# Performance work log

Measured on AMD Instinct MI355X. Metric: run time of the kernel, lower is better.

## Reference

```python
import jax, jax.numpy as jnp
from jax import lax
import numpy as np

DN = ('NCHW', 'OIHW', 'NCHW')
DL = 64
B = 1024


def _cbr(x, w, g, b, stride, pad):
    """Conv2d(bias=False) -> BatchNorm2d (training stats, eps=1e-5) -> ReLU."""
    y = lax.conv_general_dilated(x, w, (stride, stride), [(pad, pad), (pad, pad)],
                                 dimension_numbers=DN)
    m = y.mean(axis=(0, 2, 3), keepdims=True)
    v = ((y - m) ** 2).mean(axis=(0, 2, 3), keepdims=True)  # biased var, as torch BN
    y = (y - m) * lax.rsqrt(v + 1e-5)
    return jax.nn.relu(y * g[None, :, None, None] + b[None, :, None, None])


def setup_inputs() -> dict:
    key = jax.random.key(0)
    ks = jax.random.split(key, 7)
    dl = DL
    inp = {
        'x': jax.random.normal(ks[0], (B, 3, 32, 32), jnp.float32),
        'w1': jax.random.normal(ks[1], (32, 3, 3, 3), jnp.float32) * 0.1,
        'w2': jax.random.normal(ks[2], (64, 32, 3, 3), jnp.float32) * 0.05,
        'w3': jax.random.normal(ks[3], (64, 64, 3, 3), jnp.float32) * 0.05,
        'wa': jax.random.normal(ks[4], (dl, 32, 1, 1), jnp.float32) * 0.1,
        'ws1': jax.random.normal(ks[5], (3 * dl, 32, 3, 3), jnp.float32) * 0.05,
        'ws2': jax.random.normal(ks[6], (3 * dl, 3 * dl, 3, 3), jnp.float32) * 0.03,
    }
    for i, c in enumerate([32, 64, 64, dl, 3 * dl, 3 * dl]):
        inp[f'g{i}'] = jnp.ones((c,), jnp.float32)
        inp[f'b{i}'] = jnp.zeros((c,), jnp.float32)
    return inp


def _encoder(x, w1, w2, w3, wa, ws1, ws2,
             g0, b0, g1, b1, g2, b2, g3, b3, g4, b4, g5, b5):
    dl = DL
    h = _cbr(x, w1, g0, b0, 1, 1)            # [B, 32, 32, 32]
    h = _cbr(h, w2, g1, b1, 1, 1)            # [B, 64, 32, 32]
    AS = _cbr(h, w3, g2, b2, 2, 1)           # [B, 64, 16, 16]
    A_, S_ = jnp.split(AS, 2, axis=1)        # each [B, 32, 16, 16]
    A = _cbr(A_, wa, g3, b3, 1, 0)           # [B, dl, 16, 16]
    S = _cbr(S_, ws1, g4, b4, 1, 1)          # [B, 3dl, 16, 16]
    S = _cbr(S, ws2, g5, b5, 2, 1)           # [B, 3dl, 8, 8]
    b, _, ps, _ = S.shape
    S = S.reshape(b, dl, 3, ps, ps)

    # per-sample conv_transpose2d(A[ii] [1,dl,pa,pa], weight S[ii] [dl,3,ps,ps],
    # stride=2, padding=3) expressed as lhs-dilated cross-correlation with
    # flipped, channel-swapped kernel; batched via vmap (no Python loop).
    pad = ps - 1 - 3  # k - 1 - torch_padding = 4

    def ct(a, s):  # a: [dl,16,16], s: [dl,3,8,8]
        wt = jnp.flip(s, (-2, -1)).transpose(1, 0, 2, 3)  # [3, dl, 8, 8]
        return lax.conv_general_dilated(a[None], wt, (1, 1),
                                        [(pad, pad), (pad, pad)],
                                        lhs_dilation=(2, 2),
                                        dimension_numbers=DN)[0]

    recon = jax.vmap(ct)(A, S)               # [B, 3, 32, 32]
    img = jax.nn.sigmoid(x)
    recon = jax.nn.sigmoid(recon)
    l1 = jnp.mean((img - recon) ** 2)
    l2 = jnp.mean(jax.nn.relu(S))
    logp = jax.nn.log_softmax(S, axis=1)     # softmax over dl axis (dim=1)
    l3 = -jnp.mean(jnp.exp(logp) * logp)
    return A, S, 0.1 * l1, 0.1 * l2, 0.1 * l3


def reference(x, w1, w2, w3, wa, ws1, ws2,
              g0, b0, g1, b1, g2, b2, g3, b3, g4, b4, g5, b5):
    return _encoder(x, w1, w2, w3, wa, ws1, ws2,
                    g0, b0, g1, b1, g2, b2, g3, b3, g4, b4, g5, b5)
```

## Files before the change

kernel.cpp:

```cpp
#include <hip/hip_runtime.h>
#include <math.h>


typedef __attribute__((ext_vector_type(8))) short short8v;
typedef __attribute__((ext_vector_type(4))) short short4v;
typedef __attribute__((ext_vector_type(4))) float f32x4;

__device__ __forceinline__ unsigned short f2bf(float f) {
  union { float f; unsigned u; } a; a.f = f;
  unsigned r = a.u + 0x7fffu + ((a.u >> 16) & 1u);
  return (unsigned short)(r >> 16);
}
__device__ __forceinline__ float bf2f(unsigned short h) {
  union { unsigned u; float f; } a; a.u = ((unsigned)h) << 16;
  return a.f;
}

__device__ __forceinline__ float wave_reduce(float v) {
#pragma unroll
  for (int off = 32; off; off >>= 1) v += __shfl_down(v, off, 64);
  return v;
}

template <int CI, int CO>
__device__ __forceinline__ void reord1(const float* __restrict__ w,
                                       unsigned short* __restrict__ wr,
                                       int idx) {
  int e = idx & 7;
  int t = idx >> 3;
  int co = t % CO; t /= CO;
  int ci8 = t % (CI / 8);
  int kk = t / (CI / 8);
  int ci = ci8 * 8 + e;
  wr[idx] = f2bf(w[((size_t)co * CI + ci) * 9 + kk]);
}

__global__ __launch_bounds__(256) void wreord_all_k(
    const float* __restrict__ w2, const float* __restrict__ w3,
    const float* __restrict__ ws1, const float* __restrict__ ws2,
    unsigned short* __restrict__ w2r, unsigned short* __restrict__ w3r,
    unsigned short* __restrict__ ws1r, unsigned short* __restrict__ ws2r) {
  int idx = blockIdx.x * 256 + threadIdx.x;
  if (idx < 18432) reord1<32, 64>(w2, w2r, idx);
  else if (idx < 55296) reord1<64, 64>(w3, w3r, idx - 18432);
  else if (idx < 110592) reord1<32, 192>(ws1, ws1r, idx - 55296);
  else if (idx < 442368) reord1<192, 192>(ws2, ws2r, idx - 110592);
}

__global__ __launch_bounds__(256) void conv0_k(const float* __restrict__ in,
                                               const float* __restrict__ w,
                                               unsigned short* __restrict__ outB,
                                               double* __restrict__ part) {
  __shared__ __align__(16) float tile[3][34][36];
  const int b = blockIdx.x;
  const int co0 = blockIdx.y * 8;
  const int tid = threadIdx.x;
  const int row = tid >> 3, x0 = (tid & 7) * 4;
  const int wv = tid >> 6;

  float* tf = &tile[0][0][0];
  for (int i = tid; i < 918; i += 256)
    *(float4*)(tf + i * 4) = make_float4(0.f, 0.f, 0.f, 0.f);
  __syncthreads();
  for (int i = tid; i < 768; i += 256) {
    int x4 = i & 7, yy = (i >> 3) & 31, c = i >> 8;
    float4 v = *(const float4*)&in[(((size_t)b * 3 + c) * 32 + yy) * 32 + x4 * 4];
    float* dst = &tile[c][yy + 1][1 + x4 * 4];
    dst[0] = v.x; dst[1] = v.y; dst[2] = v.z; dst[3] = v.w;
  }
  __syncthreads();

  float acc[4][8];
#pragma unroll
  for (int p = 0; p < 4; ++p)
#pragma unroll
    for (int co = 0; co < 8; ++co) acc[p][co] = 0.f;

#pragma unroll
  for (int c = 0; c < 3; ++c)
#pragma unroll
    for (int ky = 0; ky < 3; ++ky) {
      const float* tr = &tile[c][row + ky][x0];
      float4 vlo = *(const float4*)tr;
      float2 vhi = *(const float2*)(tr + 4);
      float v[6] = {vlo.x, vlo.y, vlo.z, vlo.w, vhi.x, vhi.y};
#pragma unroll
      for (int kx = 0; kx < 3; ++kx)
#pragma unroll
        for (int co = 0; co < 8; ++co) {
          float wvv = w[((size_t)(co0 + co) * 3 + c) * 9 + ky * 3 + kx];
#pragma unroll
          for (int p = 0; p < 4; ++p)
            acc[p][co] = fmaf(v[p + kx], wvv, acc[p][co]);
        }
    }
#pragma unroll
  for (int p = 0; p < 4; ++p) {
    short8v o;
#pragma unroll
    for (int co = 0; co < 8; ++co) o[co] = (short)f2bf(acc[p][co]);
    *(short8v*)&outB[(((size_t)b * 32 + row) * 32 + x0 + p) * 32 + co0] = o;
  }

  float s8[8], q8[8];
#pragma unroll
  for (int co = 0; co < 8; ++co) {
    float s = 0.f, q = 0.f;
#pragma unroll
    for (int p = 0; p < 4; ++p) {
      float v = acc[p][co];
      s += v;
      q = fmaf(v, v, q);
    }
    s8[co] = wave_reduce(s);
    q8[co] = wave_reduce(q);
  }
  __syncthreads();
  float* sb = (float*)tile;
  if ((tid & 63) == 0) {
#pragma unroll
    for (int co = 0; co < 8; ++co) {
      sb[wv * 8 + co] = s8[co];
      sb[32 + wv * 8 + co] = q8[co];
    }
  }
  __syncthreads();
  if (tid < 8) {
    float S = 0.f, Q = 0.f;
#pragma unroll
    for (int k = 0; k < 4; ++k) {
      S += sb[k * 8 + tid];
      Q += sb[32 + k * 8 + tid];
    }
    size_t slot = ((size_t)(co0 + tid) * 1024 + b) * 2;
    part[slot] = (double)S;
    part[slot + 1] = (double)Q;
  }
}

template <int CI_T, int CI0, int CI, int CIP, int CO, int COB, int IHW,
          int OHW, int STRIDE, int ORPB, int WM, int WN, int CTM, int CTN,
          bool OUT_BF16T>
__global__ __launch_bounds__(512) void convgemm_k(
    const unsigned short* __restrict__ inT, const float* __restrict__ ss,
    const unsigned short* __restrict__ wr_w, float* __restrict__ outF,
    unsigned short* __restrict__ outB, double* __restrict__ part) {
  constexpr int IR = (ORPB - 1) * STRIDE + 3;
  constexpr int IW2 = IHW + 2;
  constexpr int NPX = ORPB * OHW;
  constexpr int NPIX = OHW * OHW;
  constexpr bool SWZ = (STRIDE == 2);
  static_assert(WM * WN == 8, "8 waves");
  static_assert(WN * CTN * 16 == NPX, "px tiling");
  static_assert(WM * CTM * 16 == COB, "co tiling");
  static_assert((IR * IW2 * CIP) % 4 == 0, "zero fill");
  static_assert(IR * IW2 * CIP * 2 >= 8 * CTM * 16 * 2 * 4, "stats overlay");
  static_assert(!SWZ || (CI / 8) % 8 == 0, "swizzle octet closure");
  __shared__ __align__(16) unsigned short st[IR * IW2 * CIP];

  const int b = blockIdx.x;
  const int oy0 = blockIdx.y * ORPB;
  const int co_base = blockIdx.z * COB;
  const int tid = threadIdx.x;
  const int w = tid >> 6, l = tid & 63;
  const int l16 = l & 15, g = l >> 4;
  const int wrow = w / WN, wcol = w % WN;

  {
    uint2 z = make_uint2(0u, 0u);
    uint2* stz = (uint2*)st;
    constexpr int NZ = IR * IW2 * CIP / 4;
    for (int i = tid; i < NZ; i += 512) stz[i] = z;
  }
  __syncthreads();

  {
    constexpr int CPP = CI / 8;
    constexpr int NCH = IR * IHW * CPP;
    const int r0in = oy0 * STRIDE - 1;
    for (int i = tid; i < NCH; i += 512) {
      int c8 = i % CPP;
      int xx = (i / CPP) % IHW;
      int ir = i / (CPP * IHW);
      int iy = r0in + ir;
      if ((unsigned)iy < (unsigned)IHW) {
        short8v raw = *(const short8v*)&inT[(((size_t)b * IHW + iy) * IHW + xx) *
                                            CI_T + CI0 + c8 * 8];
        f32x4 sc0 = *(const f32x4*)&ss[CI0 + c8 * 8];
        f32x4 sc1 = *(const f32x4*)&ss[CI0 + c8 * 8 + 4];
        f32x4 sh0 = *(const f32x4*)&ss[CI_T + CI0 + c8 * 8];
        f32x4 sh1 = *(const f32x4*)&ss[CI_T + CI0 + c8 * 8 + 4];
        short4v lo, hi;
#pragma unroll
        for (int e = 0; e < 4; ++e) {
          float f = bf2f((unsigned short)raw[e]);
          f = fmaxf(fmaf(f, sc0[e], sh0[e]), 0.f);
          lo[e] = (short)f2bf(f);
        }
#pragma unroll
        for (int e = 0; e < 4; ++e) {
          float f = bf2f((unsigned short)raw[e + 4]);
          f = fmaxf(fmaf(f, sc1[e], sh1[e]), 0.f);
          hi[e] = (short)f2bf(f);
        }
        int xcol = xx + 1;
        int gran = SWZ ? (c8 ^ (xcol & 7)) : c8;
        unsigned short* dst = &st[(ir * IW2 + xcol) * CIP + gran * 8];
        *(short4v*)dst = lo;
        *(short4v*)(dst + 4) = hi;
      }
    }
  }
  __syncthreads();

  int prow[CTN], pxx[CTN];
#pragma unroll
  for (int pn = 0; pn < CTN; ++pn) {
    int pxl = (wcol * CTN + pn) * 16 + l16;
    int ly = pxl / OHW, lx = pxl % OHW;
    prow[pn] = (ly * STRIDE * IW2 + lx * STRIDE) * CIP;
    pxx[pn] = lx * STRIDE;
  }
  const int co_off = co_base + wrow * CTM * 16 + l16;

  f32x4 acc[CTM][CTN];
#pragma unroll
  for (int cm = 0; cm < CTM; ++cm)
#pragma unroll
    for (int pn = 0; pn < CTN; ++pn) {
      f32x4 z = {0.f, 0.f, 0.f, 0.f};
      acc[cm][pn] = z;
    }

#pragma unroll 3
  for (int kk = 0; kk < 9; ++kk) {
    const int ky = kk / 3, kx = kk % 3;
    const int rowadd = (ky * IW2 + kx) * CIP;
#pragma unroll
    for (int cs = 0; cs < CI / 32; ++cs) {
      short8v bfr[CTN];
#pragma unroll
      for (int pn = 0; pn < CTN; ++pn) {
        int gran = cs * 4 + g;
        if (SWZ) gran ^= ((pxx[pn] + kx) & 7);
        const unsigned short* bp = &st[prow[pn] + rowadd + gran * 8];
        short4v lo = *(const short4v*)bp;
        short4v hi = *(const short4v*)(bp + 4);
        short8v v = {lo[0], lo[1], lo[2], lo[3], hi[0], hi[1], hi[2], hi[3]};
        bfr[pn] = v;
      }
      const unsigned short* wb =
          wr_w + ((size_t)(kk * (CI / 8) + cs * 4 + g) * CO + co_off) * 8;
      short8v afr[CTM];
#pragma unroll
      for (int cm = 0; cm < CTM; ++cm)
        afr[cm] = *(const short8v*)(wb + cm * 128);
#pragma unroll
      for (int cm = 0; cm < CTM; ++cm)
#pragma unroll
        for (int pn = 0; pn < CTN; ++pn)
          acc[cm][pn] = __builtin_amdgcn_mfma_f32_16x16x32_bf16(
              afr[cm], bfr[pn], acc[cm][pn], 0, 0, 0);
    }
  }

#pragma unroll
  for (int cm = 0; cm < CTM; ++cm)
#pragma unroll
    for (int pn = 0; pn < CTN; ++pn) {
      int pxl = (wcol * CTN + pn) * 16 + l16;
      size_t pxg = (size_t)oy0 * OHW + pxl;
      int co = co_base + (wrow * CTM + cm) * 16 + g * 4;
      if (OUT_BF16T) {
        unsigned d0 = (unsigned)f2bf(acc[cm][pn][0]) |
                      ((unsigned)f2bf(acc[cm][pn][1]) << 16);
        unsigned d1 = (unsigned)f2bf(acc[cm][pn][2]) |
                      ((unsigned)f2bf(acc[cm][pn][3]) << 16);
        unsigned* dst = (unsigned*)&outB[((size_t)b * NPIX + pxg) * CO + co];
        dst[0] = d0;
        dst[1] = d1;
      } else {
#pragma unroll
        for (int r = 0; r < 4; ++r)
          outF[((size_t)b * CO + co + r) * NPIX + pxg] = acc[cm][pn][r];
      }
    }

  float sst[CTM][4], qst[CTM][4];
#pragma unroll
  for (int cm = 0; cm < CTM; ++cm)
#pragma unroll
    for (int r = 0; r < 4; ++r) {
      float s = 0.f, q = 0.f;
#pragma unroll
      for (int pn = 0; pn < CTN; ++pn) {
        float v = acc[cm][pn][r];
        s += v;
        q = fmaf(v, v, q);
      }
#pragma unroll
      for (int mask = 1; mask < 16; mask <<= 1) {
        s += __shfl_xor(s, mask, 64);
        q += __shfl_xor(q, mask, 64);
      }
      sst[cm][r] = s;
      qst[cm][r] = q;
    }
  __syncthreads();
  float* sbuf = (float*)st;
  float* qbuf = sbuf + 8 * CTM * 16;
  if (l16 == 0) {
#pragma unroll
    for (int cm = 0; cm < CTM; ++cm)
#pragma unroll
      for (int r = 0; r < 4; ++r) {
        sbuf[((w * CTM + cm) * 4 + g) * 4 + r] = sst[cm][r];
        qbuf[((w * CTM + cm) * 4 + g) * 4 + r] = qst[cm][r];
      }
  }
  __syncthreads();
  if (tid < COB) {
    int wrow_t = tid / (CTM * 16);
    int rem = tid % (CTM * 16);
    float S = 0.f, Q = 0.f;
#pragma unroll
    for (int j = 0; j < WN; ++j) {
      int wvx = wrow_t * WN + j;
      S += sbuf[(wvx * CTM) * 16 + rem];
      Q += qbuf[(wvx * CTM) * 16 + rem];
    }
    const int blk = blockIdx.x * gridDim.y + blockIdx.y;
    const int nblk = 1024 * gridDim.y;
    size_t slot = ((size_t)(co_base + tid) * nblk + blk) * 2;
    part[slot] = (double)S;
    part[slot + 1] = (double)Q;
  }
}

__global__ __launch_bounds__(256) void finalize_k(
    const double* __restrict__ part, int NB, const float* __restrict__ g,
    const float* __restrict__ bb, float* __restrict__ ss, int C, double invN) {
  __shared__ double sms[256], smq[256];
  const int c = blockIdx.x;
  const int t = threadIdx.x;
  double s = 0.0, q = 0.0;
  const double* base = part + (size_t)c * NB * 2;
  for (int i = t; i < NB; i += 256) {
    s += base[i * 2];
    q += base[i * 2 + 1];
  }
  sms[t] = s;
  smq[t] = q;
  __syncthreads();
  for (int st = 128; st; st >>= 1) {
    if (t < st) {
      sms[t] += sms[t + st];
      smq[t] += smq[t + st];
    }
    __syncthreads();
  }
  if (t == 0) {
    double mean = sms[0] * invN;
    double var = smq[0] * invN - mean * mean;
    float scale = g[c] * rsqrtf((float)var + 1e-5f);
    float shift = bb[c] - (float)mean * scale;
    ss[c] = scale;
    ss[C + c] = shift;
  }
}

__global__ __launch_bounds__(256) void norm_relu_k(float* __restrict__ y,
                                                   const float* __restrict__ ss,
                                                   int C, int HW, long total) {
  long stride = (long)gridDim.x * 256 * 4;
  for (long i = ((long)blockIdx.x * 256 + threadIdx.x) * 4; i < total;
       i += stride) {
    int c = (int)((i / HW) % C);
    float sc = ss[c], sh = ss[C + c];
    float4 v = *(const float4*)(y + i);
    v.x = fmaxf(fmaf(v.x, sc, sh), 0.f);
    v.y = fmaxf(fmaf(v.y, sc, sh), 0.f);
    v.z = fmaxf(fmaf(v.z, sc, sh), 0.f);
    v.w = fmaxf(fmaf(v.w, sc, sh), 0.f);
    *(float4*)(y + i) = v;
  }
}

__global__ __launch_bounds__(256) void conv1x1_k(
    const unsigned short* __restrict__ inT, const float* __restrict__ ss,
    const float* __restrict__ w, float* __restrict__ out,
    double* __restrict__ part) {
  __shared__ float sb1x[4][16], qb1x[4][16];
  const int b = blockIdx.x;
  const int co0 = blockIdx.y * 16;
  const int px = threadIdx.x;
  const int wv = threadIdx.x >> 6;
  float acc[16];
#pragma unroll
  for (int co = 0; co < 16; ++co) acc[co] = 0.f;
  const unsigned short* rowp = inT + ((size_t)b * 256 + px) * 64;
#pragma unroll
  for (int c8 = 0; c8 < 4; ++c8) {
    short8v raw = *(const short8v*)(rowp + c8 * 8);
#pragma unroll
    for (int e = 0; e < 8; ++e) {
      int c = c8 * 8 + e;
      float f = bf2f((unsigned short)raw[e]);
      f = fmaxf(fmaf(f, ss[c], ss[64 + c]), 0.f);
#pragma unroll
      for (int co = 0; co < 16; ++co)
        acc[co] = fmaf(f, w[(co0 + co) * 32 + c], acc[co]);
    }
  }
#pragma unroll
  for (int co = 0; co < 16; ++co)
    out[((size_t)b * 64 + co0 + co) * 256 + px] = acc[co];

#pragma unroll
  for (int co = 0; co < 16; ++co) {
    float s = wave_reduce(acc[co]);
    float q = wave_reduce(acc[co] * acc[co]);
    if ((threadIdx.x & 63) == 0) {
      sb1x[wv][co] = s;
      qb1x[wv][co] = q;
    }
  }
  __syncthreads();
  if (px < 16) {
    float S = 0.f, Q = 0.f;
#pragma unroll
    for (int k = 0; k < 4; ++k) {
      S += sb1x[k][px];
      Q += qb1x[k][px];
    }
    size_t slot = ((size_t)(co0 + px) * 1024 + b) * 2;
    part[slot] = (double)S;
    part[slot + 1] = (double)Q;
  }
}

__global__ __launch_bounds__(256) void convt_l1_k(const float* __restrict__ A,
                                                  const float* __restrict__ S,
                                                  const float* __restrict__ x,
                                                  double* __restrict__ l1p) {
  __shared__ unsigned short Ab[8][256][8];
  __shared__ unsigned short Sb[4][16][3][72];
  __shared__ float sbred[4];
  const int b = blockIdx.x, tid = threadIdx.x;
  const int w = tid >> 6, l = tid & 63;
  const int g = l >> 4, c = l & 15;
  const int pa = w >> 1, pb = w & 1;

  const float* Ag = A + (size_t)b * 16384;
  for (int dp = 0; dp < 32; ++dp) {
    int d = dp * 2;
    unsigned lo = f2bf(Ag[(size_t)d * 256 + tid]);
    unsigned hi = f2bf(Ag[(size_t)(d + 1) * 256 + tid]);
    *(unsigned*)&Ab[d >> 3][tid][d & 7] = lo | (hi << 16);
  }
  const float* Sg = S + (size_t)b * 12288;
  for (int i = tid; i < 12288; i += 256) {
    int cch = i >> 6;
    int tap = i & 63;
    int d = cch / 3, t = cch - 3 * d;
    int ky = tap >> 3, kx = tap & 7;
    int par = (((ky & 1) ^ 1) << 1) | ((kx & 1) ^ 1);
    Sb[par][(ky >> 1) * 4 + (kx >> 1)][t][d] = f2bf(Sg[i]);
  }
  __syncthreads();

  f32x4 acc[16];
#pragma unroll
  for (int nt = 0; nt < 16; ++nt) {
    f32x4 z = {0.f, 0.f, 0.f, 0.f};
    acc[nt] = z;
  }

  const int shy = 1 + pa, shx = 1 + pb;
  for (int s = 0; s < 32; ++s) {
    const int tap = s >> 1;
    const int m = tap >> 2, n = tap & 3;
    const int dh = s & 1;
    short8v afr = {0, 0, 0, 0, 0, 0, 0, 0};
    if (c < 3) afr = *(const short8v*)&Sb[w][tap][c][dh * 32 + g * 8];
    const int ix = c + shx - n;
    const bool xok = (unsigned)ix < 16u;
    const int dblk = dh * 4 + g;
#pragma unroll
    for (int nt = 0; nt < 16; ++nt) {
      int iy = nt + shy - m;
      if ((unsigned)iy >= 16u) continue;
      short8v bfr = {0, 0, 0, 0, 0, 0, 0, 0};
      if (xok) bfr = *(const short8v*)&Ab[dblk][iy * 16 + ix][0];
      acc[nt] = __builtin_amdgcn_mfma_f32_16x16x32_bf16(afr, bfr, acc[nt],
                                                        0, 0, 0);
    }
  }

  float loc = 0.f;
  if (g == 0) {
    const float* xg = x + (size_t)b * 3072;
#pragma unroll
    for (int nt = 0; nt < 16; ++nt) {
      int oy = 2 * nt + pa, ox = 2 * c + pb;
#pragma unroll
      for (int r = 0; r < 3; ++r) {
        float recon = 1.f / (1.f + expf(-acc[nt][r]));
        float img = 1.f / (1.f + expf(-xg[r * 1024 + oy * 32 + ox]));
        float dd = img - recon;
        loc = fmaf(dd, dd, loc);
      }
    }
  }
  loc = wave_reduce(loc);
  if (l == 0) sbred[w] = loc;
  __syncthreads();
  if (tid == 0)
    l1p[b] = (double)(sbred[0] + sbred[1] + sbred[2] + sbred[3]);
}

__global__ __launch_bounds__(256) void loss23_k(const float* __restrict__ S,
                                                double* __restrict__ l2p,
                                                double* __restrict__ l3p) {
  __shared__ float sb1[4], sb2[4];
  int gid = blockIdx.x * 256 + threadIdx.x;
  int b = gid / 192;
  int r = gid - b * 192;
  int t = r >> 6, p = r & 63;
  const float* base = S + ((size_t)b * 192 + t) * 64 + p;
  float v[64];
  float l2 = 0.f, m = -1e30f;
#pragma unroll
  for (int d = 0; d < 64; ++d) {
    v[d] = base[(size_t)d * 192];
    m = fmaxf(m, v[d]);
    l2 += fmaxf(v[d], 0.f);
  }
  float Z = 0.f;
#pragma unroll
  for (int d = 0; d < 64; ++d) Z += expf(v[d] - m);
  float lZ = logf(Z);
  float l3 = 0.f;
#pragma unroll
  for (int d = 0; d < 64; ++d) {
    float lp = v[d] - m - lZ;
    l3 = fmaf(expf(lp), lp, l3);
  }
  l2 = wave_reduce(l2);
  l3 = wave_reduce(l3);
  int lane = threadIdx.x & 63, w = threadIdx.x >> 6;
  if (lane == 0) { sb1[w] = l2; sb2[w] = l3; }
  __syncthreads();
  if (threadIdx.x == 0) {
    l2p[blockIdx.x] = (double)(sb1[0] + sb1[1] + sb1[2] + sb1[3]);
    l3p[blockIdx.x] = (double)(sb2[0] + sb2[1] + sb2[2] + sb2[3]);
  }
}

__global__ __launch_bounds__(256) void scalars_k(const double* __restrict__ l1p,
                                                 const double* __restrict__ l2p,
                                                 const double* __restrict__ l3p,
                                                 float* __restrict__ out) {
  __shared__ double sm[256];
  const int t = threadIdx.x;

  double a = 0.0;
  for (int i = t; i < 1024; i += 256) a += l1p[i];
  sm[t] = a;
  __syncthreads();
  for (int s = 128; s; s >>= 1) {
    if (t < s) sm[t] += sm[t + s];
    __syncthreads();
  }
  double L1 = sm[0];
  __syncthreads();

  a = 0.0;
  for (int i = t; i < 768; i += 256) a += l2p[i];
  sm[t] = a;
  __syncthreads();
  for (int s = 128; s; s >>= 1) {
    if (t < s) sm[t] += sm[t + s];
    __syncthreads();
  }
  double L2 = sm[0];
  __syncthreads();

  a = 0.0;
  for (int i = t; i < 768; i += 256) a += l3p[i];
  sm[t] = a;
  __syncthreads();
  for (int s = 128; s; s >>= 1) {
    if (t < s) sm[t] += sm[t + s];
    __syncthreads();
  }
  double L3 = sm[0];

  if (t == 0) {
    out[0] = (float)(0.1 * L1 / 3145728.0);
    out[1] = (float)(0.1 * L2 / 12582912.0);
    out[2] = (float)(-0.1 * L3 / 12582912.0);
  }
}

extern "C" void kernel_launch(void* const* d_in, const int* in_sizes, int n_in,
                              void* d_out, int out_size, void* d_ws,
                              size_t ws_size, hipStream_t stream) {
  const float* x = (const float*)d_in[0];
  const float* w1 = (const float*)d_in[1];
  const float* w2 = (const float*)d_in[2];
  const float* w3 = (const float*)d_in[3];
  const float* wa = (const float*)d_in[4];
  const float* ws1 = (const float*)d_in[5];
  const float* ws2 = (const float*)d_in[6];
  const float* gb[12];
  for (int i = 0; i < 12; ++i) gb[i] = (const float*)d_in[7 + i];

  float* dout = (float*)d_out;
  float* Aout = dout;
  float* Sout = dout + 16777216LL;
  float* sc_out = dout + 29360128LL;

  float* wsf = (float*)d_ws;
  unsigned short* y1b = (unsigned short*)(wsf);
  unsigned short* y2b = (unsigned short*)(wsf + 16777216LL);
  unsigned short* y3b = (unsigned short*)(wsf + 50331648LL);
  unsigned short* y5b = (unsigned short*)(wsf + 58720256LL);
  unsigned short* wts = (unsigned short*)(wsf + 83886080LL);
  unsigned short* w2r = wts;
  unsigned short* w3r = wts + 18432;
  unsigned short* ws1r = wts + 55296;
  unsigned short* ws2r = wts + 110592;
  double* part = (double*)(wsf + 84107264LL);
  double* l1p = (double*)(wsf + 85680128LL);
  double* l2p = l1p + 1024;
  double* l3p = l2p + 768;
  float* ssL = (float*)(l3p + 768);
  float* ss0 = ssL, *ss1 = ssL + 384, *ss2 = ssL + 768;
  float* ss3 = ssL + 1152, *ss4 = ssL + 1536, *ss5 = ssL + 1920;

  wreord_all_k<<<1728, 256, 0, stream>>>(w2, w3, ws1, ws2, w2r, w3r, ws1r, ws2r);

  conv0_k<<<dim3(1024, 4), 256, 0, stream>>>(x, w1, y1b, part);
  finalize_k<<<32, 256, 0, stream>>>(part, 1024, gb[0], gb[1], ss0, 32, 1.0 / 1048576.0);

  convgemm_k<32, 0, 32, 36, 64, 64, 32, 32, 1, 8, 2, 4, 2, 4, true>
      <<<dim3(1024, 4, 1), 512, 0, stream>>>(y1b, ss0, w2r, nullptr, y2b, part);
  finalize_k<<<64, 256, 0, stream>>>(part, 4096, gb[2], gb[3], ss1, 64, 1.0 / 1048576.0);

  convgemm_k<64, 0, 64, 68, 64, 64, 32, 16, 2, 8, 2, 4, 2, 2, true>
      <<<dim3(1024, 2, 1), 512, 0, stream>>>(y2b, ss1, w3r, nullptr, y3b, part);
  finalize_k<<<64, 256, 0, stream>>>(part, 2048, gb[4], gb[5], ss2, 64, 1.0 / 262144.0);

  conv1x1_k<<<dim3(1024, 4), 256, 0, stream>>>(y3b, ss2, wa, Aout, part);
  finalize_k<<<64, 256, 0, stream>>>(part, 1024, gb[6], gb[7], ss3, 64, 1.0 / 262144.0);
  norm_relu_k<<<4096, 256, 0, stream>>>(Aout, ss3, 64, 256, 16777216L);

  convgemm_k<64, 32, 32, 36, 192, 96, 16, 16, 1, 16, 2, 4, 3, 4, true>
      <<<dim3(1024, 1, 2), 512, 0, stream>>>(y3b, ss2, ws1r, nullptr, y5b, part);
  finalize_k<<<192, 256, 0, stream>>>(part, 1024, gb[8], gb[9], ss4, 192, 1.0 / 262144.0);

  convgemm_k<192, 0, 192, 196, 192, 192, 16, 8, 2, 4, 4, 2, 3, 1, false>
      <<<dim3(1024, 2, 1), 512, 0, stream>>>(y5b, ss4, ws2r, Sout, nullptr, part);
  finalize_k<<<192, 256, 0, stream>>>(part, 2048, gb[10], gb[11], ss5, 192, 1.0 / 65536.0);
  norm_relu_k<<<4096, 256, 0, stream>>>(Sout, ss5, 192, 64, 12582912L);

  convt_l1_k<<<1024, 256, 0, stream>>>(Aout, Sout, x, l1p);
  loss23_k<<<768, 256, 0, stream>>>(Sout, l2p, l3p);
  scalars_k<<<1, 256, 0, stream>>>(l1p, l2p, l3p, sc_out);
}
```

Measured before the change: 671.4 us.

## Fuse BN-ReLU epilogues into loss kernels and swizzle half-granule LDS stores

The two standalone norm_relu passes over A and S are removed. The scale/shift/ReLU is now applied inside loss23_k, which also writes S back, and inside convt_l1_k, which writes A back. loss23_k is launched first so that S is already normalised when convt_l1_k reads it. This saves a full read-write pass over roughly 29M floats. Separately, the conv LDS tile swaps its 4-element halves according to column parity, aiming to reduce bank conflicts in the split short4 loads and stores.

```diff
diff --git a/kernel.cpp b/kernel.cpp
--- a/kernel.cpp
+++ b/kernel.cpp
@@ -205,9 +205,10 @@
         }
         int xcol = xx + 1;
         int gran = SWZ ? (c8 ^ (xcol & 7)) : c8;
+        int pp = SWZ ? ((xcol >> 1) & 1) : 0;
         unsigned short* dst = &st[(ir * IW2 + xcol) * CIP + gran * 8];
-        *(short4v*)dst = lo;
-        *(short4v*)(dst + 4) = hi;
+        *(short4v*)(dst + 4 * pp) = lo;
+        *(short4v*)(dst + 4 * (1 - pp)) = hi;
       }
     }
   }
@@ -241,11 +242,16 @@
       short8v bfr[CTN];
 #pragma unroll
       for (int pn = 0; pn < CTN; ++pn) {
+        int col = pxx[pn] + kx;
         int gran = cs * 4 + g;
-        if (SWZ) gran ^= ((pxx[pn] + kx) & 7);
+        int pp = 0;
+        if (SWZ) {
+          gran ^= (col & 7);
+          pp = (col >> 1) & 1;
+        }
         const unsigned short* bp = &st[prow[pn] + rowadd + gran * 8];
-        short4v lo = *(const short4v*)bp;
-        short4v hi = *(const short4v*)(bp + 4);
+        short4v lo = *(const short4v*)(bp + 4 * pp);
+        short4v hi = *(const short4v*)(bp + 4 * (1 - pp));
         short8v v = {lo[0], lo[1], lo[2], lo[3], hi[0], hi[1], hi[2], hi[3]};
         bfr[pn] = v;
       }
@@ -369,23 +375,6 @@
   }
 }
 
-__global__ __launch_bounds__(256) void norm_relu_k(float* __restrict__ y,
-                                                   const float* __restrict__ ss,
-                                                   int C, int HW, long total) {
-  long stride = (long)gridDim.x * 256 * 4;
-  for (long i = ((long)blockIdx.x * 256 + threadIdx.x) * 4; i < total;
-       i += stride) {
-    int c = (int)((i / HW) % C);
-    float sc = ss[c], sh = ss[C + c];
-    float4 v = *(const float4*)(y + i);
-    v.x = fmaxf(fmaf(v.x, sc, sh), 0.f);
-    v.y = fmaxf(fmaf(v.y, sc, sh), 0.f);
-    v.z = fmaxf(fmaf(v.z, sc, sh), 0.f);
-    v.w = fmaxf(fmaf(v.w, sc, sh), 0.f);
-    *(float4*)(y + i) = v;
-  }
-}
-
 __global__ __launch_bounds__(256) void conv1x1_k(
     const unsigned short* __restrict__ inT, const float* __restrict__ ss,
     const float* __restrict__ w, float* __restrict__ out,
@@ -439,9 +428,10 @@
   }
 }
 
-__global__ __launch_bounds__(256) void convt_l1_k(const float* __restrict__ A,
+__global__ __launch_bounds__(256) void convt_l1_k(float* __restrict__ A,
                                                   const float* __restrict__ S,
                                                   const float* __restrict__ x,
+                                                  const float* __restrict__ ssA,
                                                   double* __restrict__ l1p) {
   __shared__ unsigned short Ab[8][256][8];
   __shared__ unsigned short Sb[4][16][3][72];
@@ -451,11 +441,17 @@
   const int g = l >> 4, c = l & 15;
   const int pa = w >> 1, pb = w & 1;
 
-  const float* Ag = A + (size_t)b * 16384;
+  float* Ag = A + (size_t)b * 16384;
   for (int dp = 0; dp < 32; ++dp) {
     int d = dp * 2;
-    unsigned lo = f2bf(Ag[(size_t)d * 256 + tid]);
-    unsigned hi = f2bf(Ag[(size_t)(d + 1) * 256 + tid]);
+    float f0 = Ag[(size_t)d * 256 + tid];
+    float f1 = Ag[(size_t)(d + 1) * 256 + tid];
+    f0 = fmaxf(fmaf(f0, ssA[d], ssA[64 + d]), 0.f);
+    f1 = fmaxf(fmaf(f1, ssA[d + 1], ssA[64 + d + 1]), 0.f);
+    Ag[(size_t)d * 256 + tid] = f0;
+    Ag[(size_t)(d + 1) * 256 + tid] = f1;
+    unsigned lo = f2bf(f0);
+    unsigned hi = f2bf(f1);
     *(unsigned*)&Ab[d >> 3][tid][d & 7] = lo | (hi << 16);
   }
   const float* Sg = S + (size_t)b * 12288;
@@ -519,23 +515,32 @@
     l1p[b] = (double)(sbred[0] + sbred[1] + sbred[2] + sbred[3]);
 }
 
-__global__ __launch_bounds__(256) void loss23_k(const float* __restrict__ S,
+__global__ __launch_bounds__(256) void loss23_k(float* __restrict__ S,
+                                                const float* __restrict__ ss,
                                                 double* __restrict__ l2p,
                                                 double* __restrict__ l3p) {
+  __shared__ float ssl[384];
   __shared__ float sb1[4], sb2[4];
+  for (int i = threadIdx.x; i < 384; i += 256) ssl[i] = ss[i];
+  __syncthreads();
   int gid = blockIdx.x * 256 + threadIdx.x;
   int b = gid / 192;
   int r = gid - b * 192;
   int t = r >> 6, p = r & 63;
-  const float* base = S + ((size_t)b * 192 + t) * 64 + p;
+  float* base = S + ((size_t)b * 192 + t) * 64 + p;
   float v[64];
   float l2 = 0.f, m = -1e30f;
 #pragma unroll
   for (int d = 0; d < 64; ++d) {
-    v[d] = base[(size_t)d * 192];
-    m = fmaxf(m, v[d]);
-    l2 += fmaxf(v[d], 0.f);
-  }
+    float raw = base[(size_t)d * 192];
+    int cch = d * 3 + t;
+    float f = fmaxf(fmaf(raw, ssl[cch], ssl[192 + cch]), 0.f);
+    v[d] = f;
+    m = fmaxf(m, f);
+    l2 += f;
+  }
+#pragma unroll
+  for (int d = 0; d < 64; ++d) base[(size_t)d * 192] = v[d];
   float Z = 0.f;
 #pragma unroll
   for (int d = 0; d < 64; ++d) Z += expf(v[d] - m);
@@ -654,7 +659,6 @@
 
   conv1x1_k<<<dim3(1024, 4), 256, 0, stream>>>(y3b, ss2, wa, Aout, part);
   finalize_k<<<64, 256, 0, stream>>>(part, 1024, gb[6], gb[7], ss3, 64, 1.0 / 262144.0);
-  norm_relu_k<<<4096, 256, 0, stream>>>(Aout, ss3, 64, 256, 16777216L);
 
   convgemm_k<64, 32, 32, 36, 192, 96, 16, 16, 1, 16, 2, 4, 3, 4, true>
       <<<dim3(1024, 1, 2), 512, 0, stream>>>(y3b, ss2, ws1r, nullptr, y5b, part);
@@ -663,9 +667,8 @@
   convgemm_k<192, 0, 192, 196, 192, 192, 16, 8, 2, 4, 4, 2, 3, 1, false>
       <<<dim3(1024, 2, 1), 512, 0, stream>>>(y5b, ss4, ws2r, Sout, nullptr, part);
   finalize_k<<<192, 256, 0, stream>>>(part, 2048, gb[10], gb[11], ss5, 192, 1.0 / 65536.0);
-  norm_relu_k<<<4096, 256, 0, stream>>>(Sout, ss5, 192, 64, 12582912L);
-
-  convt_l1_k<<<1024, 256, 0, stream>>>(Aout, Sout, x, l1p);
-  loss23_k<<<768, 256, 0, stream>>>(Sout, l2p, l3p);
+
+  loss23_k<<<768, 256, 0, stream>>>(Sout, ss5, l2p, l3p);
+  convt_l1_k<<<1024, 256, 0, stream>>>(Aout, Sout, x, ss3, l1p);
   scalars_k<<<1, 256, 0, stream>>>(l1p, l2p, l3p, sc_out);
 }
```

Result: no change. 676.4 us (+0.7%).
